# Optimization experiments

Measured on AMD Instinct MI355X. Metric: run time of the kernel, lower is better.

## Reference

```python
import jax, jax.numpy as jnp
import numpy as np


def _grid_sample_3d(src, grid):
    """Trilinear grid_sample, align_corners=True, zero padding.
    src: [B,C,D,H,W], grid: [B,D,H,W,3] with last dim (x,y,z) ~ (W,H,D) in [-1,1].
    """
    B, C, D, H, W = src.shape
    gx, gy, gz = grid[..., 0], grid[..., 1], grid[..., 2]
    # unnormalize (align_corners=True): -1 -> 0, +1 -> dim-1
    ix = (gx + 1.0) * ((W - 1) / 2.0)
    iy = (gy + 1.0) * ((H - 1) / 2.0)
    iz = (gz + 1.0) * ((D - 1) / 2.0)
    ix0 = jnp.floor(ix); iy0 = jnp.floor(iy); iz0 = jnp.floor(iz)
    fx = ix - ix0; fy = iy - iy0; fz = iz - iz0  # fractional parts
    x0 = ix0.astype(jnp.int32); y0 = iy0.astype(jnp.int32); z0 = iz0.astype(jnp.int32)

    src_flat = src.reshape(B, C, D * H * W)
    out = jnp.zeros((B, C, D * H * W), dtype=src.dtype)
    for dz in (0, 1):
        for dy in (0, 1):
            for dx in (0, 1):
                xc = x0 + dx; yc = y0 + dy; zc = z0 + dz
                w = ((fx if dx else 1.0 - fx)
                     * (fy if dy else 1.0 - fy)
                     * (fz if dz else 1.0 - fz))
                valid = ((xc >= 0) & (xc < W) & (yc >= 0) & (yc < H)
                         & (zc >= 0) & (zc < D))
                xs = jnp.clip(xc, 0, W - 1)
                ys = jnp.clip(yc, 0, H - 1)
                zs = jnp.clip(zc, 0, D - 1)
                lin = ((zs * H + ys) * W + xs).reshape(B, -1)  # [B, DHW]
                vals = jax.vmap(lambda s, i: jnp.take(s, i, axis=1))(src_flat, lin)  # [B,C,DHW]
                out = out + (w * valid).reshape(B, 1, -1).astype(src.dtype) * vals
    return out.reshape(B, C, D, H, W)


def _affine_grid_3d(theta, D, H, W):
    """torch affine_grid (align_corners=True) for size [B,3,D,H,W]. Returns [B,D,H,W,3]."""
    xs = jnp.linspace(-1.0, 1.0, W, dtype=theta.dtype)
    ys = jnp.linspace(-1.0, 1.0, H, dtype=theta.dtype)
    zs = jnp.linspace(-1.0, 1.0, D, dtype=theta.dtype)
    bx = jnp.broadcast_to(xs[None, None, :], (D, H, W))
    by = jnp.broadcast_to(ys[None, :, None], (D, H, W))
    bz = jnp.broadcast_to(zs[:, None, None], (D, H, W))
    base = jnp.stack([bx, by, bz, jnp.ones((D, H, W), theta.dtype)], axis=-1)  # [D,H,W,4]
    return jnp.einsum('bij,dhwj->bdhwi', theta, base)


def setup_inputs() -> dict:
    key = jax.random.key(0)
    k1, k2 = jax.random.split(key)
    B, C, D, H, W = 2, 2, 160, 192, 224
    src = jax.random.normal(k1, (B, C, D, H, W), dtype=jnp.float32)
    eye = jnp.concatenate([jnp.eye(3, dtype=jnp.float32),
                           jnp.zeros((3, 1), jnp.float32)], axis=1)  # [3,4]
    mat = eye[None] + 0.05 * jax.random.normal(k2, (B, 3, 4), dtype=jnp.float32)
    return {"src": src, "mat": mat}


def reference(src, mat):
    B, C, D, H, W = src.shape
    norm = jnp.array([[1, 1, 1, D], [1, 1, 1, H], [1, 1, 1, W]], dtype=mat.dtype)
    theta = mat / norm[None]  # normalize translation column by spatial dims
    grid = _affine_grid_3d(theta, D, H, W)
    return _grid_sample_3d(src, grid)
```

## Files before the change

### kernel.cpp

```cpp
#include <hip/hip_runtime.h>

#define BB 2
#define CC 2
#define DD 160
#define HH 192
#define WW 224
#define DHW (DD * HH * WW)

#define VPT 4
#define QD  (DD / VPT)
#define QOFF (QD * HH * WW)
#define TPB 256
#define NBX (QOFF / TPB)
#define NXCD 8
#define CPX (NBX / NXCD)

typedef float f2v __attribute__((ext_vector_type(2)));

__device__ __forceinline__ f2v load2u(const float* p) {
    struct __attribute__((packed)) S { f2v v; };
    return ((const S*)p)->v;
}

__global__ __launch_bounds__(TPB, 4) void affine_sample_kernel(
    const float* __restrict__ src,
    const float* __restrict__ mat,
    float* __restrict__ out)
{
    int bx  = blockIdx.x;
    int sbx = (bx & (NXCD - 1)) * CPX + (bx >> 3);
    int base = sbx * TPB + (int)threadIdx.x;
    int b = blockIdx.y;

    int w = base % WW;
    int t = base / WW;
    int h = t % HH;
    int d = t / HH;

    const float* m = mat + b * 12;
    float a00 = m[0], a01 = m[1], a02 = m[2],  a03 = m[3]  * (1.0f / (float)DD);
    float a10 = m[4], a11 = m[5], a12 = m[6],  a13 = m[7]  * (1.0f / (float)HH);
    float a20 = m[8], a21 = m[9], a22 = m[10], a23 = m[11] * (1.0f / (float)WW);

    float xn = -1.0f + (float)w * (2.0f / (float)(WW - 1));
    float yn = -1.0f + (float)h * (2.0f / (float)(HH - 1));
    float zn = -1.0f + (float)d * (2.0f / (float)(DD - 1));

    float ix = (a00 * xn + a01 * yn + a02 * zn + a03 + 1.0f) * ((float)(WW - 1) * 0.5f);
    float iy = (a10 * xn + a11 * yn + a12 * zn + a13 + 1.0f) * ((float)(HH - 1) * 0.5f);
    float iz = (a20 * xn + a21 * yn + a22 * zn + a23 + 1.0f) * ((float)(DD - 1) * 0.5f);

    float dzn = (float)QD * (2.0f / (float)(DD - 1));
    float dix = a02 * dzn * ((float)(WW - 1) * 0.5f);
    float diy = a12 * dzn * ((float)(HH - 1) * 0.5f);
    float diz = a22 * dzn * ((float)(DD - 1) * 0.5f);

    const float* s0 = src + (size_t)b * (CC * DHW);
    const float* s1 = s0 + DHW;

    f2v   P0[VPT][4], P1[VPT][4];
    float q0a[VPT], q1a[VPT];
    float wzy0[VPT], wzy1[VPT], wzy2[VPT], wzy3[VPT];

    #pragma unroll
    for (int v = 0; v < VPT; ++v) {
        float ixv = fmaf((float)v, dix, ix);
        float iyv = fmaf((float)v, diy, iy);
        float izv = fmaf((float)v, diz, iz);

        float fx0 = floorf(ixv), fy0 = floorf(iyv), fz0 = floorf(izv);
        float fx = ixv - fx0, fy = iyv - fy0, fz = izv - fz0;
        int x0 = (int)fx0, y0 = (int)fy0, z0 = (int)fz0;
        int x1 = x0 + 1, y1 = y0 + 1, z1 = z0 + 1;

        float wx0 = (x0 >= 0 && x0 < WW) ? (1.0f - fx) : 0.0f;
        float wx1 = (x1 >= 0 && x1 < WW) ? fx          : 0.0f;
        float wy0 = (y0 >= 0 && y0 < HH) ? (1.0f - fy) : 0.0f;
        float wy1 = (y1 >= 0 && y1 < HH) ? fy          : 0.0f;
        float wz0 = (z0 >= 0 && z0 < DD) ? (1.0f - fz) : 0.0f;
        float wz1 = (z1 >= 0 && z1 < DD) ? fz          : 0.0f;

        int xc0 = min(max(x0, 0), WW - 1), xc1 = min(max(x1, 0), WW - 1);
        int yc0 = min(max(y0, 0), HH - 1), yc1 = min(max(y1, 0), HH - 1);
        int zc0 = min(max(z0, 0), DD - 1), zc1 = min(max(z1, 0), DD - 1);

        int xb   = min(xc0, WW - 2);
        int sel0 = xc0 - xb;
        int sel1 = xc1 - xb;

        q0a[v] = (sel0 ? 0.0f : wx0) + (sel1 ? 0.0f : wx1);
        q1a[v] = (sel0 ? wx0 : 0.0f) + (sel1 ? wx1 : 0.0f);

        wzy0[v] = wz0 * wy0; wzy1[v] = wz0 * wy1;
        wzy2[v] = wz1 * wy0; wzy3[v] = wz1 * wy1;

        int zh0 = zc0 * HH, zh1 = zc1 * HH;
        int r0 = (zh0 + yc0) * WW + xb;
        int r1 = (zh0 + yc1) * WW + xb;
        int r2 = (zh1 + yc0) * WW + xb;
        int r3 = (zh1 + yc1) * WW + xb;

        P0[v][0] = load2u(s0 + r0);
        P0[v][1] = load2u(s0 + r1);
        P0[v][2] = load2u(s0 + r2);
        P0[v][3] = load2u(s0 + r3);
        P1[v][0] = load2u(s1 + r0);
        P1[v][1] = load2u(s1 + r1);
        P1[v][2] = load2u(s1 + r2);
        P1[v][3] = load2u(s1 + r3);
    }

    __builtin_amdgcn_sched_barrier(0);

    float* o = out + (size_t)b * (CC * DHW) + base;
    #pragma unroll
    for (int v = 0; v < VPT; ++v) {
        float rq00 = wzy0[v] * q0a[v], rq01 = wzy0[v] * q1a[v];
        float rq10 = wzy1[v] * q0a[v], rq11 = wzy1[v] * q1a[v];
        float rq20 = wzy2[v] * q0a[v], rq21 = wzy2[v] * q1a[v];
        float rq30 = wzy3[v] * q0a[v], rq31 = wzy3[v] * q1a[v];

        float acc0 = rq00 * P0[v][0][0] + rq01 * P0[v][0][1]
                   + rq10 * P0[v][1][0] + rq11 * P0[v][1][1]
                   + rq20 * P0[v][2][0] + rq21 * P0[v][2][1]
                   + rq30 * P0[v][3][0] + rq31 * P0[v][3][1];
        float acc1 = rq00 * P1[v][0][0] + rq01 * P1[v][0][1]
                   + rq10 * P1[v][1][0] + rq11 * P1[v][1][1]
                   + rq20 * P1[v][2][0] + rq21 * P1[v][2][1]
                   + rq30 * P1[v][3][0] + rq31 * P1[v][3][1];

        __builtin_nontemporal_store(acc0, o + v * QOFF);
        __builtin_nontemporal_store(acc1, o + (DHW + v * QOFF));
    }
}

extern "C" void kernel_launch(void* const* d_in, const int* in_sizes, int n_in,
                              void* d_out, int out_size, void* d_ws, size_t ws_size,
                              hipStream_t stream) {
    const float* src = (const float*)d_in[0];
    const float* mat = (const float*)d_in[1];
    float* out = (float*)d_out;

    dim3 block(TPB);
    dim3 grid(NBX, BB);
    affine_sample_kernel<<<grid, block, 0, stream>>>(src, mat, out);
}
```

Measured before the change: 243.7 us.

## Tile work as 2-row by 8-slice z-columns per block for cache reuse

Each block now covers two full W-rows and each thread walks 8 consecutive z-slices, where before each thread handled 4 voxels spaced a quarter-volume apart. Adjacent z outputs share source neighbours, so this aims to improve L1/L2 reuse of the gathered 2x2x2 stencils. The gather-all-then-compute split and its sched_barrier are removed, and loads and math are interleaved per slice, which lowers register pressure but may expose more memory latency. Blocks become 448 threads, and the occupancy hint in the launch bounds is dropped.

```diff
diff --git a/kernel.cpp b/kernel.cpp
--- a/kernel.cpp
+++ b/kernel.cpp
@@ -6,12 +6,14 @@
 #define HH 192
 #define WW 224
 #define DHW (DD * HH * WW)
+#define HW  (HH * WW)
 
-#define VPT 4
-#define QD  (DD / VPT)
-#define QOFF (QD * HH * WW)
-#define TPB 256
-#define NBX (QOFF / TPB)
+#define ZT 8
+#define HT 2
+#define TPB (WW * HT)
+#define NH (HH / HT)
+#define NZ (DD / ZT)
+#define NBX (NH * NZ)
 #define NXCD 8
 #define CPX (NBX / NXCD)
 
@@ -22,51 +24,49 @@
     return ((const S*)p)->v;
 }
 
-__global__ __launch_bounds__(TPB, 4) void affine_sample_kernel(
+__global__ __launch_bounds__(TPB) void affine_sample_kernel(
     const float* __restrict__ src,
     const float* __restrict__ mat,
     float* __restrict__ out)
 {
     int bx  = blockIdx.x;
     int sbx = (bx & (NXCD - 1)) * CPX + (bx >> 3);
-    int base = sbx * TPB + (int)threadIdx.x;
-    int b = blockIdx.y;
+    int h2  = sbx % NH;
+    int z8  = sbx / NH;
+    int b   = blockIdx.y;
 
-    int w = base % WW;
-    int t = base / WW;
-    int h = t % HH;
-    int d = t / HH;
+    int tid = (int)threadIdx.x;
+    int w   = tid % WW;
+    int h   = h2 * HT + tid / WW;
+    int d0  = z8 * ZT;
 
     const float* m = mat + b * 12;
     float a00 = m[0], a01 = m[1], a02 = m[2],  a03 = m[3]  * (1.0f / (float)DD);
     float a10 = m[4], a11 = m[5], a12 = m[6],  a13 = m[7]  * (1.0f / (float)HH);
     float a20 = m[8], a21 = m[9], a22 = m[10], a23 = m[11] * (1.0f / (float)WW);
 
-    float xn = -1.0f + (float)w * (2.0f / (float)(WW - 1));
-    float yn = -1.0f + (float)h * (2.0f / (float)(HH - 1));
-    float zn = -1.0f + (float)d * (2.0f / (float)(DD - 1));
+    float xn = -1.0f + (float)w  * (2.0f / (float)(WW - 1));
+    float yn = -1.0f + (float)h  * (2.0f / (float)(HH - 1));
+    float zn = -1.0f + (float)d0 * (2.0f / (float)(DD - 1));
 
-    float ix = (a00 * xn + a01 * yn + a02 * zn + a03 + 1.0f) * ((float)(WW - 1) * 0.5f);
-    float iy = (a10 * xn + a11 * yn + a12 * zn + a13 + 1.0f) * ((float)(HH - 1) * 0.5f);
-    float iz = (a20 * xn + a21 * yn + a22 * zn + a23 + 1.0f) * ((float)(DD - 1) * 0.5f);
+    float ix0 = (a00 * xn + a01 * yn + a02 * zn + a03 + 1.0f) * ((float)(WW - 1) * 0.5f);
+    float iy0 = (a10 * xn + a11 * yn + a12 * zn + a13 + 1.0f) * ((float)(HH - 1) * 0.5f);
+    float iz0 = (a20 * xn + a21 * yn + a22 * zn + a23 + 1.0f) * ((float)(DD - 1) * 0.5f);
 
-    float dzn = (float)QD * (2.0f / (float)(DD - 1));
+    float dzn = 2.0f / (float)(DD - 1);
     float dix = a02 * dzn * ((float)(WW - 1) * 0.5f);
     float diy = a12 * dzn * ((float)(HH - 1) * 0.5f);
     float diz = a22 * dzn * ((float)(DD - 1) * 0.5f);
 
     const float* s0 = src + (size_t)b * (CC * DHW);
     const float* s1 = s0 + DHW;
-
-    f2v   P0[VPT][4], P1[VPT][4];
-    float q0a[VPT], q1a[VPT];
-    float wzy0[VPT], wzy1[VPT], wzy2[VPT], wzy3[VPT];
+    float* o = out + (size_t)b * (CC * DHW) + (d0 * HH + h) * WW + w;
 
     #pragma unroll
-    for (int v = 0; v < VPT; ++v) {
-        float ixv = fmaf((float)v, dix, ix);
-        float iyv = fmaf((float)v, diy, iy);
-        float izv = fmaf((float)v, diz, iz);
+    for (int v = 0; v < ZT; ++v) {
+        float ixv = fmaf((float)v, dix, ix0);
+        float iyv = fmaf((float)v, diy, iy0);
+        float izv = fmaf((float)v, diz, iz0);
 
         float fx0 = floorf(ixv), fy0 = floorf(iyv), fz0 = floorf(izv);
         float fx = ixv - fx0, fy = iyv - fy0, fz = izv - fz0;
@@ -88,11 +88,11 @@
         int sel0 = xc0 - xb;
         int sel1 = xc1 - xb;
 
-        q0a[v] = (sel0 ? 0.0f : wx0) + (sel1 ? 0.0f : wx1);
-        q1a[v] = (sel0 ? wx0 : 0.0f) + (sel1 ? wx1 : 0.0f);
+        float q0 = (sel0 ? 0.0f : wx0) + (sel1 ? 0.0f : wx1);
+        float q1 = (sel0 ? wx0 : 0.0f) + (sel1 ? wx1 : 0.0f);
 
-        wzy0[v] = wz0 * wy0; wzy1[v] = wz0 * wy1;
-        wzy2[v] = wz1 * wy0; wzy3[v] = wz1 * wy1;
+        float w00 = wz0 * wy0, w01 = wz0 * wy1;
+        float w10 = wz1 * wy0, w11 = wz1 * wy1;
 
         int zh0 = zc0 * HH, zh1 = zc1 * HH;
         int r0 = (zh0 + yc0) * WW + xb;
@@ -100,37 +100,31 @@
         int r2 = (zh1 + yc0) * WW + xb;
         int r3 = (zh1 + yc1) * WW + xb;
 
-        P0[v][0] = load2u(s0 + r0);
-        P0[v][1] = load2u(s0 + r1);
-        P0[v][2] = load2u(s0 + r2);
-        P0[v][3] = load2u(s0 + r3);
-        P1[v][0] = load2u(s1 + r0);
-        P1[v][1] = load2u(s1 + r1);
-        P1[v][2] = load2u(s1 + r2);
-        P1[v][3] = load2u(s1 + r3);
-    }
+        f2v pa0 = load2u(s0 + r0);
+        f2v pa1 = load2u(s0 + r1);
+        f2v pa2 = load2u(s0 + r2);
+        f2v pa3 = load2u(s0 + r3);
+        f2v pb0 = load2u(s1 + r0);
+        f2v pb1 = load2u(s1 + r1);
+        f2v pb2 = load2u(s1 + r2);
+        f2v pb3 = load2u(s1 + r3);
 
-    __builtin_amdgcn_sched_barrier(0);
+        float rq00 = w00 * q0, rq01 = w00 * q1;
+        float rq10 = w01 * q0, rq11 = w01 * q1;
+        float rq20 = w10 * q0, rq21 = w10 * q1;
+        float rq30 = w11 * q0, rq31 = w11 * q1;
 
-    float* o = out + (size_t)b * (CC * DHW) + base;
-    #pragma unroll
-    for (int v = 0; v < VPT; ++v) {
-        float rq00 = wzy0[v] * q0a[v], rq01 = wzy0[v] * q1a[v];
-        float rq10 = wzy1[v] * q0a[v], rq11 = wzy1[v] * q1a[v];
-        float rq20 = wzy2[v] * q0a[v], rq21 = wzy2[v] * q1a[v];
-        float rq30 = wzy3[v] * q0a[v], rq31 = wzy3[v] * q1a[v];
+        float acc0 = rq00 * pa0[0] + rq01 * pa0[1]
+                   + rq10 * pa1[0] + rq11 * pa1[1]
+                   + rq20 * pa2[0] + rq21 * pa2[1]
+                   + rq30 * pa3[0] + rq31 * pa3[1];
+        float acc1 = rq00 * pb0[0] + rq01 * pb0[1]
+                   + rq10 * pb1[0] + rq11 * pb1[1]
+                   + rq20 * pb2[0] + rq21 * pb2[1]
+                   + rq30 * pb3[0] + rq31 * pb3[1];
 
-        float acc0 = rq00 * P0[v][0][0] + rq01 * P0[v][0][1]
-                   + rq10 * P0[v][1][0] + rq11 * P0[v][1][1]
-                   + rq20 * P0[v][2][0] + rq21 * P0[v][2][1]
-                   + rq30 * P0[v][3][0] + rq31 * P0[v][3][1];
-        float acc1 = rq00 * P1[v][0][0] + rq01 * P1[v][0][1]
-                   + rq10 * P1[v][1][0] + rq11 * P1[v][1][1]
-                   + rq20 * P1[v][2][0] + rq21 * P1[v][2][1]
-                   + rq30 * P1[v][3][0] + rq31 * P1[v][3][1];
-
-        __builtin_nontemporal_store(acc0, o + v * QOFF);
-        __builtin_nontemporal_store(acc1, o + (DHW + v * QOFF));
+        __builtin_nontemporal_store(acc0, o + v * HW);
+        __builtin_nontemporal_store(acc1, o + (DHW + v * HW));
     }
 }
 
```

Result: slower. 263.8 us (+8.2%).
